# Kernel tuning notes

Hardware: AMD Instinct MI355X
Metric: run time of the kernel (lower is better)

Reference implementation:

```python
import jax, jax.numpy as jnp
import numpy as np

NUM_HEADS = 4
NUM_GROUPS = 8
EPS = 1e-5


def group_norm(x, w, b):
    # x: [B, C, H, W], 8 groups, per-channel affine
    B, C, H, W = x.shape
    g = x.reshape(B, NUM_GROUPS, C // NUM_GROUPS, H, W)
    mu = g.mean(axis=(2, 3, 4), keepdims=True)
    var = g.var(axis=(2, 3, 4), keepdims=True)
    g = (g - mu) * jax.lax.rsqrt(var + EPS)
    x = g.reshape(B, C, H, W)
    return x * w[None, :, None, None] + b[None, :, None, None]


def setup_inputs() -> dict:
    key = jax.random.key(0)
    ks = jax.random.split(key, 7)
    B, C, H, W = 16, 256, 32, 32
    x = jax.random.normal(ks[0], (B, C, H, W), dtype=jnp.float32)
    norm_w = jnp.ones((C,), jnp.float32)
    norm_b = jnp.zeros((C,), jnp.float32)
    # 1x1 convs == channel matmuls; fan-in scaled init
    qkv_w = jax.random.normal(ks[1], (3 * C, C), dtype=jnp.float32) / np.sqrt(C)
    qkv_b = jnp.zeros((3 * C,), jnp.float32)
    proj_w = jax.random.normal(ks[2], (C, C), dtype=jnp.float32) / np.sqrt(C)
    proj_b = jnp.zeros((C,), jnp.float32)
    return {"x": x, "norm_w": norm_w, "norm_b": norm_b,
            "qkv_w": qkv_w, "qkv_b": qkv_b,
            "proj_w": proj_w, "proj_b": proj_b}


def reference(x, norm_w, norm_b, qkv_w, qkv_b, proj_w, proj_b):
    B, C, H, W = x.shape
    nh = NUM_HEADS
    d = C // nh
    N = H * W

    h = group_norm(x, norm_w, norm_b)
    # 1x1 conv -> channel matmul: [B, 3C, H, W]
    qkv = jnp.einsum('oc,bchw->bohw', qkv_w, h) + qkv_b[None, :, None, None]
    qkv = qkv.reshape(B, 3, nh, d, N)
    q, k, v = qkv[:, 0], qkv[:, 1], qkv[:, 2]  # [B, nh, d, N]

    scale = d ** (-0.5)
    attn = jnp.einsum('bhcn,bhcm->bhnm', q, k) * scale  # [B, nh, N, N]
    attn = jax.nn.softmax(attn, axis=-1)
    out = jnp.einsum('bhnm,bhcm->bhcn', attn, v)  # [B, nh, d, N]
    out = out.reshape(B, C, H, W)
    out = jnp.einsum('oc,bchw->bohw', proj_w, out) + proj_b[None, :, None, None]
    return x + out
```

## Files before the change

### kernel.cpp

```cpp
#include <hip/hip_runtime.h>
#include <math.h>

#define BATCH 16
#define CH 256
#define NG 8
#define NH 4
#define HD 64
#define NN 1024
#define GSZ 32
#define GELEMS (GSZ * NN)

typedef __attribute__((ext_vector_type(8))) __bf16 bf16x8;
typedef __attribute__((ext_vector_type(4))) __bf16 bf16x4;
typedef __attribute__((ext_vector_type(4))) float f32x4;

__device__ __forceinline__ unsigned short f2b(float f) {
    union { __bf16 h; unsigned short u; } c; c.h = (__bf16)f; return c.u;
}

#define MFMA(a, b, c) __builtin_amdgcn_mfma_f32_16x16x32_bf16(a, b, c, 0, 0, 0)

__global__ __launch_bounds__(256) void prep_kernel(
    const float* __restrict__ x, const float* __restrict__ qkv_w,
    const float* __restrict__ proj_w, float* __restrict__ stats,
    unsigned short* __restrict__ wq, unsigned short* __restrict__ wp)
{
    int tid = threadIdx.x;
    if (blockIdx.x >= 128) {
        int t = (blockIdx.x - 128) * 256 + tid;
        const float* src; unsigned short* dst; size_t off;
        if (t < 24576) { src = qkv_w; dst = wq; off = (size_t)t * 8; }
        else           { src = proj_w; dst = wp; off = (size_t)(t - 24576) * 8; }
        const float4* s4 = (const float4*)(src + off);
        float4 a = s4[0], b = s4[1];
        bf16x8 pk;
        pk[0] = (__bf16)a.x; pk[1] = (__bf16)a.y; pk[2] = (__bf16)a.z; pk[3] = (__bf16)a.w;
        pk[4] = (__bf16)b.x; pk[5] = (__bf16)b.y; pk[6] = (__bf16)b.z; pk[7] = (__bf16)b.w;
        *(bf16x8*)(dst + off) = pk;
        return;
    }
    int b = blockIdx.x >> 3, g = blockIdx.x & 7;
    const float4* x4 = (const float4*)(x + ((size_t)b * CH + g * GSZ) * NN);
    float s = 0.f, ss = 0.f;
    #pragma unroll
    for (int i = 0; i < 32; ++i) {
        float4 v = x4[tid + i * 256];
        s  += v.x + v.y + v.z + v.w;
        ss += v.x * v.x + v.y * v.y + v.z * v.z + v.w * v.w;
    }
    #pragma unroll
    for (int off = 1; off < 64; off <<= 1) {
        s  += __shfl_xor(s, off);
        ss += __shfl_xor(ss, off);
    }
    __shared__ float red[8];
    int wave = tid >> 6, lane = tid & 63;
    if (lane == 0) { red[wave] = s; red[4 + wave] = ss; }
    __syncthreads();
    if (tid == 0) {
        float ts  = red[0] + red[1] + red[2] + red[3];
        float tss = red[4] + red[5] + red[6] + red[7];
        float mu  = ts * (1.f / GELEMS);
        float var = tss * (1.f / GELEMS) - mu * mu;
        stats[blockIdx.x * 2] = mu;
        stats[blockIdx.x * 2 + 1] = rsqrtf(var + 1e-5f);
    }
}

__global__ __launch_bounds__(256) void gn_apply_kernel(
    const float* __restrict__ x, const float* __restrict__ w,
    const float* __restrict__ bb, const float* __restrict__ stats,
    unsigned short* __restrict__ hT)
{
    __shared__ float Ts[64][68];
    __shared__ float wcp[256], bcp[256];
    const int b = blockIdx.y, n0 = blockIdx.x * 64;
    const int tid = threadIdx.x;
    {
        int c = tid, g = c >> 5;
        float mu = stats[(b * 8 + g) * 2], rs = stats[(b * 8 + g) * 2 + 1];
        float wc = w[c] * rs;
        wcp[c] = wc; bcp[c] = bb[c] - mu * wc;
    }
    __syncthreads();
    const float* xb = x + (size_t)b * CH * NN;
    const int c_l = tid >> 2, nq = tid & 3;
    const int n_l = tid >> 2, cq = tid & 3;
    for (int cb = 0; cb < 4; ++cb) {
        #pragma unroll
        for (int i = 0; i < 4; ++i)
            *(float4*)&Ts[c_l][nq * 4 + i * 16] =
                *(const float4*)(xb + (size_t)(cb * 64 + c_l) * NN + n0 + nq * 4 + i * 16);
        __syncthreads();
        #pragma unroll
        for (int s = 0; s < 2; ++s) {
            int cbase = cq * 16 + s * 8;
            bf16x8 pk;
            #pragma unroll
            for (int j = 0; j < 8; ++j) {
                int c = cb * 64 + cbase + j;
                pk[j] = (__bf16)(Ts[cbase + j][n_l] * wcp[c] + bcp[c]);
            }
            *(bf16x8*)(hT + ((size_t)b * NN + n0 + n_l) * CH + cb * 64 + cbase) = pk;
        }
        __syncthreads();
    }
}

template <int KIND>
__global__ __launch_bounds__(256) void gemm_kernel(
    const unsigned short* __restrict__ AT,
    const unsigned short* __restrict__ Wb,
    const float* __restrict__ bias,
    unsigned short* __restrict__ outT, unsigned short* __restrict__ outV,
    const float* __restrict__ res, float* __restrict__ out)
{
    __shared__ __align__(16) unsigned short Ws[64][136];
    __shared__ __align__(16) unsigned short Hs[64][136];
    const int b = blockIdx.z, o0 = blockIdx.y * 64, n0 = blockIdx.x * 64;
    const int tid = threadIdx.x;
    const int lane = tid & 63, wv = tid >> 6;
    const int l = lane & 15, quad = lane >> 4;
    const int iw = wv & 1, jw = wv >> 1;
    const bool qk_mode = (KIND == 0) && (blockIdx.y < 8);
    const int r4 = tid >> 2, c4 = tid & 3;

    f32x4 acc[2][2] = {};
    for (int st = 0; st < 2; ++st) {
        const int cc0 = st * 128;
        #pragma unroll
        for (int i = 0; i < 4; ++i) {
            int ch = c4 + i * 4;
            *(bf16x8*)&Ws[r4][ch * 8] =
                *(const bf16x8*)(Wb + (size_t)(o0 + r4) * CH + cc0 + ch * 8);
            *(bf16x8*)&Hs[r4][ch * 8] =
                *(const bf16x8*)(AT + ((size_t)b * NN + n0 + r4) * CH + cc0 + ch * 8);
        }
        __syncthreads();
        #pragma unroll
        for (int kt = 0; kt < 4; ++kt) {
            bf16x8 af[2], bf[2];
            #pragma unroll
            for (int i = 0; i < 2; ++i)
                af[i] = *(const bf16x8*)&Hs[iw * 32 + i * 16 + l][kt * 32 + quad * 8];
            #pragma unroll
            for (int j = 0; j < 2; ++j)
                bf[j] = *(const bf16x8*)&Ws[jw * 32 + j * 16 + l][kt * 32 + quad * 8];
            #pragma unroll
            for (int i = 0; i < 2; ++i)
                #pragma unroll
                for (int j = 0; j < 2; ++j)
                    acc[i][j] = qk_mode ? MFMA(af[i], bf[j], acc[i][j])
                                        : MFMA(bf[j], af[i], acc[i][j]);
        }
        __syncthreads();
    }

    #pragma unroll
    for (int i = 0; i < 2; ++i)
        #pragma unroll
        for (int j = 0; j < 2; ++j) {
            if (qk_mode) {
                int o = o0 + jw * 32 + j * 16 + l;
                float bs = bias[o];
                #pragma unroll
                for (int r = 0; r < 4; ++r) {
                    int n = n0 + iw * 32 + i * 16 + quad * 4 + r;
                    outT[((size_t)b * NN + n) * 512 + o] = f2b(acc[i][j][r] + bs);
                }
            } else {
                int o = o0 + jw * 32 + j * 16 + quad * 4;
                int n = n0 + iw * 32 + i * 16 + l;
                #pragma unroll
                for (int r = 0; r < 4; ++r) {
                    float v = acc[i][j][r] + bias[o + r];
                    if (KIND == 0)
                        outV[((size_t)b * CH + (o + r - 512)) * NN + n] = f2b(v);
                    else {
                        size_t idx = ((size_t)b * CH + o + r) * NN + n;
                        out[idx] = v + res[idx];
                    }
                }
            }
        }
}

__global__ __launch_bounds__(256) void attn_kernel(
    const unsigned short* __restrict__ qkvT,
    const unsigned short* __restrict__ vbuf,
    unsigned short* __restrict__ ctxT)
{
    __shared__ __align__(16) unsigned short Qs[64][72];
    __shared__ __align__(16) unsigned short Ks[64][72];
    __shared__ __align__(16) unsigned short Vs[64][72];
    __shared__ __align__(16) unsigned short Ps[64][72];
    __shared__ float Ls[64];
    const int n0 = blockIdx.x * 64, hh = blockIdx.y, b = blockIdx.z;
    const int tid = threadIdx.x;
    const int lane = tid & 63, wv = tid >> 6;
    const int l = lane & 15, quad = lane >> 4;
    const float KL2E = 0.125f * 1.44269504f;
    const int r4 = tid >> 2, c4 = tid & 3;

    #pragma unroll
    for (int i = 0; i < 2; ++i) {
        int ch = c4 + i * 4;
        *(bf16x8*)&Qs[r4][ch * 8] =
            *(const bf16x8*)(qkvT + ((size_t)b * NN + n0 + r4) * 512 + hh * HD + ch * 8);
    }
    bf16x8 qf[2];
    #pragma unroll
    for (int kt = 0; kt < 2; ++kt)
        qf[kt] = *(const bf16x8*)&Qs[wv * 16 + l][kt * 32 + quad * 8];

    float l_part = 0.f;
    f32x4 oacc[4] = {};

    for (int mt = 0; mt < 16; ++mt) {
        const int m0 = mt * 64;
        #pragma unroll
        for (int i = 0; i < 2; ++i) {
            int ch = c4 + i * 4;
            *(bf16x8*)&Ks[r4][ch * 8] =
                *(const bf16x8*)(qkvT + ((size_t)b * NN + m0 + r4) * 512 + 256 + hh * HD + ch * 8);
            *(bf16x8*)&Vs[r4][ch * 8] =
                *(const bf16x8*)(vbuf + ((size_t)b * CH + hh * HD + r4) * NN + m0 + ch * 8);
        }
        __syncthreads();

        f32x4 sacc[4] = {};
        #pragma unroll
        for (int kt = 0; kt < 2; ++kt) {
            #pragma unroll
            for (int ct = 0; ct < 4; ++ct) {
                bf16x8 kf = *(const bf16x8*)&Ks[ct * 16 + l][kt * 32 + quad * 8];
                sacc[ct] = MFMA(kf, qf[kt], sacc[ct]);
            }
        }
        #pragma unroll
        for (int ct = 0; ct < 4; ++ct) {
            bf16x4 pk;
            #pragma unroll
            for (int r = 0; r < 4; ++r) {
                float p = exp2f(sacc[ct][r] * KL2E);
                l_part += p;
                pk[r] = (__bf16)p;
            }
            *(bf16x4*)&Ps[wv * 16 + l][ct * 16 + quad * 4] = pk;
        }
        #pragma unroll
        for (int kt = 0; kt < 2; ++kt) {
            bf16x8 pa = *(const bf16x8*)&Ps[wv * 16 + l][kt * 32 + quad * 8];
            #pragma unroll
            for (int ct = 0; ct < 4; ++ct) {
                bf16x8 vv = *(const bf16x8*)&Vs[ct * 16 + l][kt * 32 + quad * 8];
                oacc[ct] = MFMA(pa, vv, oacc[ct]);
            }
        }
        __syncthreads();
    }

    l_part += __shfl_xor(l_part, 16);
    l_part += __shfl_xor(l_part, 32);
    if (quad == 0) Ls[wv * 16 + l] = l_part;
    float inv[4];
    #pragma unroll
    for (int r = 0; r < 4; ++r) inv[r] = 1.f / Ls[wv * 16 + quad * 4 + r];
    #pragma unroll
    for (int ct = 0; ct < 4; ++ct)
        #pragma unroll
        for (int r = 0; r < 4; ++r)
            ctxT[((size_t)b * NN + n0 + wv * 16 + quad * 4 + r) * CH + hh * HD + ct * 16 + l] =
                f2b(oacc[ct][r] * inv[r]);
}

extern "C" void kernel_launch(void* const* d_in, const int* in_sizes, int n_in,
                              void* d_out, int out_size, void* d_ws, size_t ws_size,
                              hipStream_t stream)
{
    const float* x      = (const float*)d_in[0];
    const float* norm_w = (const float*)d_in[1];
    const float* norm_b = (const float*)d_in[2];
    const float* qkv_w  = (const float*)d_in[3];
    const float* qkv_b  = (const float*)d_in[4];
    const float* proj_w = (const float*)d_in[5];
    const float* proj_b = (const float*)d_in[6];
    float* out = (float*)d_out;

    unsigned short* hT   = (unsigned short*)d_ws;
    unsigned short* qkvT = hT   + (size_t)BATCH * NN * CH;
    unsigned short* vbuf = qkvT + (size_t)BATCH * NN * 512;
    unsigned short* ctxT = vbuf + (size_t)BATCH * CH * NN;
    unsigned short* wq   = ctxT + (size_t)BATCH * NN * CH;
    unsigned short* wp   = wq + (size_t)768 * CH;
    float* stats         = (float*)(wp + (size_t)CH * CH);

    prep_kernel<<<dim3(256), 256, 0, stream>>>(x, qkv_w, proj_w, stats, wq, wp);
    gn_apply_kernel<<<dim3(16, BATCH), 256, 0, stream>>>(x, norm_w, norm_b, stats, hT);
    gemm_kernel<0><<<dim3(NN / 64, 12, BATCH), 256, 0, stream>>>(
        hT, wq, qkv_b, qkvT, vbuf, nullptr, nullptr);
    attn_kernel<<<dim3(NN / 64, NH, BATCH), 256, 0, stream>>>(qkvT, vbuf, ctxT);
    gemm_kernel<1><<<dim3(NN / 64, 4, BATCH), 256, 0, stream>>>(
        ctxT, wp, proj_b, nullptr, nullptr, x, out);
}
```

Measured before the change: 150.4 us.

## Restructure attention: 2x2 wave split over queries and keys with direct-to-LDS loads

```diff
diff --git a/kernel.cpp b/kernel.cpp
--- a/kernel.cpp
+++ b/kernel.cpp
@@ -19,6 +19,12 @@
 }
 
 #define MFMA(a, b, c) __builtin_amdgcn_mfma_f32_16x16x32_bf16(a, b, c, 0, 0, 0)
+
+typedef __attribute__((address_space(1))) unsigned int ga_u32;
+typedef __attribute__((address_space(3))) unsigned int ls_u32;
+__device__ __forceinline__ void dma16(const void* g, void* l) {
+    __builtin_amdgcn_global_load_lds((ga_u32*)g, (ls_u32*)l, 16, 0, 0);
+}
 
 __global__ __launch_bounds__(256) void prep_kernel(
     const float* __restrict__ x, const float* __restrict__ qkv_w,
@@ -190,88 +196,126 @@
     const unsigned short* __restrict__ vbuf,
     unsigned short* __restrict__ ctxT)
 {
-    __shared__ __align__(16) unsigned short Qs[64][72];
-    __shared__ __align__(16) unsigned short Ks[64][72];
-    __shared__ __align__(16) unsigned short Vs[64][72];
-    __shared__ __align__(16) unsigned short Ps[64][72];
-    __shared__ float Ls[64];
+    __shared__ __align__(16) unsigned short KV[8192];
+    __shared__ __align__(16) unsigned short Ps[4][32][36];
+    __shared__ float Lred[2][2][32];
     const int n0 = blockIdx.x * 64, hh = blockIdx.y, b = blockIdx.z;
     const int tid = threadIdx.x;
-    const int lane = tid & 63, wv = tid >> 6;
+    const int lane = tid & 63, w = tid >> 6;
     const int l = lane & 15, quad = lane >> 4;
+    const int qx = w & 1, ky = w >> 1;
     const float KL2E = 0.125f * 1.44269504f;
-    const int r4 = tid >> 2, c4 = tid & 3;
-
-    #pragma unroll
-    for (int i = 0; i < 2; ++i) {
-        int ch = c4 + i * 4;
-        *(bf16x8*)&Qs[r4][ch * 8] =
-            *(const bf16x8*)(qkvT + ((size_t)b * NN + n0 + r4) * 512 + hh * HD + ch * 8);
-    }
-    bf16x8 qf[2];
-    #pragma unroll
-    for (int kt = 0; kt < 2; ++kt)
-        qf[kt] = *(const bf16x8*)&Qs[wv * 16 + l][kt * 32 + quad * 8];
-
-    float l_part = 0.f;
-    f32x4 oacc[4] = {};
+
+    const int drow = lane >> 3;
+    const int dchunk = (lane & 7) ^ (drow & 7);
+
+    bf16x8 qf[2][2];
+    {
+        const unsigned short* qp = qkvT + ((size_t)b * NN + n0 + 32 * qx + l) * 512 + hh * 64;
+        #pragma unroll
+        for (int ns = 0; ns < 2; ++ns)
+            #pragma unroll
+            for (int kt = 0; kt < 2; ++kt)
+                qf[ns][kt] = *(const bf16x8*)(qp + (size_t)ns * 16 * 512 + kt * 32 + quad * 8);
+    }
+
+    float l_w[2] = {0.f, 0.f};
+    f32x4 oacc[2][4] = {};
 
     for (int mt = 0; mt < 16; ++mt) {
         const int m0 = mt * 64;
         #pragma unroll
-        for (int i = 0; i < 2; ++i) {
-            int ch = c4 + i * 4;
-            *(bf16x8*)&Ks[r4][ch * 8] =
-                *(const bf16x8*)(qkvT + ((size_t)b * NN + m0 + r4) * 512 + 256 + hh * HD + ch * 8);
-            *(bf16x8*)&Vs[r4][ch * 8] =
-                *(const bf16x8*)(vbuf + ((size_t)b * CH + hh * HD + r4) * NN + m0 + ch * 8);
-        }
-        __syncthreads();
-
-        f32x4 sacc[4] = {};
-        #pragma unroll
-        for (int kt = 0; kt < 2; ++kt) {
+        for (int s = 0; s < 2; ++s) {
+            int rb = (w * 2 + s) * 8;
+            const unsigned short* gk = qkvT + ((size_t)b * NN + m0 + rb + drow) * 512
+                                       + 256 + hh * 64 + dchunk * 8;
+            dma16(gk, &KV[rb * 64]);
+            const unsigned short* gv = vbuf + ((size_t)b * CH + hh * 64 + rb + drow) * NN
+                                       + m0 + dchunk * 8;
+            dma16(gv, &KV[4096 + rb * 64]);
+        }
+        __syncthreads();
+
+        f32x4 sacc[2][2] = {};
+        #pragma unroll
+        for (int kt = 0; kt < 2; ++kt)
+            #pragma unroll
+            for (int mt2 = 0; mt2 < 2; ++mt2) {
+                int r = 32 * ky + 16 * mt2 + l;
+                bf16x8 kf = *(const bf16x8*)&KV[r * 64 + (((kt * 4 + quad) ^ (l & 7)) * 8)];
+                #pragma unroll
+                for (int ns = 0; ns < 2; ++ns)
+                    sacc[mt2][ns] = MFMA(kf, qf[ns][kt], sacc[mt2][ns]);
+            }
+
+        #pragma unroll
+        for (int ns = 0; ns < 2; ++ns)
+            #pragma unroll
+            for (int mt2 = 0; mt2 < 2; ++mt2) {
+                bf16x4 pk;
+                #pragma unroll
+                for (int r = 0; r < 4; ++r) {
+                    float p = exp2f(sacc[mt2][ns][r] * KL2E);
+                    l_w[ns] += p;
+                    pk[r] = (__bf16)p;
+                }
+                *(bf16x4*)&Ps[w][ns * 16 + l][mt2 * 16 + quad * 4] = pk;
+            }
+
+        #pragma unroll
+        for (int ns = 0; ns < 2; ++ns) {
+            bf16x8 pa = *(const bf16x8*)&Ps[w][ns * 16 + l][quad * 8];
             #pragma unroll
             for (int ct = 0; ct < 4; ++ct) {
-                bf16x8 kf = *(const bf16x8*)&Ks[ct * 16 + l][kt * 32 + quad * 8];
-                sacc[ct] = MFMA(kf, qf[kt], sacc[ct]);
-            }
-        }
-        #pragma unroll
-        for (int ct = 0; ct < 4; ++ct) {
-            bf16x4 pk;
-            #pragma unroll
-            for (int r = 0; r < 4; ++r) {
-                float p = exp2f(sacc[ct][r] * KL2E);
-                l_part += p;
-                pk[r] = (__bf16)p;
-            }
-            *(bf16x4*)&Ps[wv * 16 + l][ct * 16 + quad * 4] = pk;
-        }
-        #pragma unroll
-        for (int kt = 0; kt < 2; ++kt) {
-            bf16x8 pa = *(const bf16x8*)&Ps[wv * 16 + l][kt * 32 + quad * 8];
-            #pragma unroll
-            for (int ct = 0; ct < 4; ++ct) {
-                bf16x8 vv = *(const bf16x8*)&Vs[ct * 16 + l][kt * 32 + quad * 8];
-                oacc[ct] = MFMA(pa, vv, oacc[ct]);
-            }
-        }
-        __syncthreads();
-    }
-
-    l_part += __shfl_xor(l_part, 16);
-    l_part += __shfl_xor(l_part, 32);
-    if (quad == 0) Ls[wv * 16 + l] = l_part;
-    float inv[4];
+                int r = 16 * ct + l;
+                bf16x8 vv = *(const bf16x8*)&KV[4096 + r * 64 + (((ky * 4 + quad) ^ (l & 7)) * 8)];
+                oacc[ns][ct] = MFMA(pa, vv, oacc[ns][ct]);
+            }
+        }
+        __syncthreads();
+    }
+
     #pragma unroll
-    for (int r = 0; r < 4; ++r) inv[r] = 1.f / Ls[wv * 16 + quad * 4 + r];
-    #pragma unroll
-    for (int ct = 0; ct < 4; ++ct)
-        #pragma unroll
-        for (int r = 0; r < 4; ++r)
-            ctxT[((size_t)b * NN + n0 + wv * 16 + quad * 4 + r) * CH + hh * HD + ct * 16 + l] =
-                f2b(oacc[ct][r] * inv[r]);
+    for (int ns = 0; ns < 2; ++ns) {
+        l_w[ns] += __shfl_xor(l_w[ns], 16);
+        l_w[ns] += __shfl_xor(l_w[ns], 32);
+    }
+    __syncthreads();
+    float* Ored = (float*)KV;
+    if (ky == 1) {
+        #pragma unroll
+        for (int ns = 0; ns < 2; ++ns) {
+            if (quad == 0) Lred[0][qx][ns * 16 + l] = l_w[ns];
+            #pragma unroll
+            for (int ct = 0; ct < 4; ++ct)
+                #pragma unroll
+                for (int r = 0; r < 4; ++r)
+                    Ored[qx * 2048 + (ns * 16 + quad * 4 + r) * 64 + ct * 16 + l] = oacc[ns][ct][r];
+        }
+    }
+    __syncthreads();
+    if (ky == 0) {
+        #pragma unroll
+        for (int ns = 0; ns < 2; ++ns)
+            if (quad == 0)
+                Lred[1][qx][ns * 16 + l] = l_w[ns] + Lred[0][qx][ns * 16 + l];
+        unsigned short* cb = ctxT + ((size_t)b * NN + n0 + 32 * qx) * CH + hh * 64;
+        #pragma unroll
+        for (int ns = 0; ns < 2; ++ns) {
+            float inv[4];
+            #pragma unroll
+            for (int r = 0; r < 4; ++r)
+                inv[r] = 1.f / Lred[1][qx][ns * 16 + quad * 4 + r];
+            #pragma unroll
+            for (int ct = 0; ct < 4; ++ct)
+                #pragma unroll
+                for (int r = 0; r < 4; ++r) {
+                    float o = oacc[ns][ct][r] +
+                              Ored[qx * 2048 + (ns * 16 + quad * 4 + r) * 64 + ct * 16 + l];
+                    cb[(size_t)(ns * 16 + quad * 4 + r) * CH + ct * 16 + l] = f2b(o * inv[r]);
+                }
+        }
+    }
 }
 
 extern "C" void kernel_launch(void* const* d_in, const int* in_sizes, int n_in,
@@ -299,7 +343,7 @@
     gn_apply_kernel<<<dim3(16, BATCH), 256, 0, stream>>>(x, norm_w, norm_b, stats, hT);
     gemm_kernel<0><<<dim3(NN / 64, 12, BATCH), 256, 0, stream>>>(
         hT, wq, qkv_b, qkvT, vbuf, nullptr, nullptr);
-    attn_kernel<<<dim3(NN / 64, NH, BATCH), 256, 0, stream>>>(qkvT, vbuf, ctxT);
+    attn_kernel<<<dim3(16, NH, BATCH), 256, 0, stream>>>(qkvT, vbuf, ctxT);
     gemm_kernel<1><<<dim3(NN / 64, 4, BATCH), 256, 0, stream>>>(
         ctxT, wp, proj_b, nullptr, nullptr, x, out);
 }
```

Result: slower. 156.5 us (+4.1%).
